# Optimization experiments

Hardware: AMD Instinct MI355X
Metric: run time of the kernel (lower is better)

Reference implementation:

```python
import jax, jax.numpy as jnp
import numpy as np

N = 100000
E = 640000
C = 128
NEG_SLOPE = 0.2


def _param(key, shape, scale=0.1):
    return jax.random.normal(key, shape, dtype=jnp.float32) * scale


def setup_inputs() -> dict:
    key = jax.random.key(0)
    ks = jax.random.split(key, 20)
    edge_index = jax.random.randint(ks[0], (2, E), 0, N, dtype=jnp.int32)
    emb = jax.random.normal(ks[1], (N, C), dtype=jnp.float32)  # node_embeddings.weight, a=1.0 normal
    d = {"edge_index": edge_index, "emb": emb}
    # per-layer GATv2Conv params: lin_l (W,b), lin_r (W,b), att vector, residual lin (no bias), out bias
    names = ["Wl", "bl", "Wr", "br", "att", "Wres", "bias"]
    shapes = [(C, C), (C,), (C, C), (C,), (C,), (C, C), (C,)]
    i = 2
    for layer in (1, 2):
        for nm, sh in zip(names, shapes):
            d[f"l{layer}_{nm}"] = _param(ks[i], sh)
            i += 1
    return d


def gatv2_layer(x, Wl, bl, Wr, br, att, Wres, bias, src, dst):
    # x: [N,C]; src/dst: [E+N] (self loops included)
    xl = x @ Wl.T + bl                       # source-side transform [N,C]
    xr = x @ Wr.T + br                       # target-side transform [N,C]
    m = jax.nn.leaky_relu(xl[src] + xr[dst], NEG_SLOPE)  # [E',C]
    e = m @ att                               # attention logits [E']
    emax = jax.ops.segment_max(e, dst, num_segments=N)
    ex = jnp.exp(e - emax[dst])
    denom = jax.ops.segment_sum(ex, dst, num_segments=N)
    alpha = ex / denom[dst]                   # segment softmax over incoming edges
    out = jax.ops.segment_sum(alpha[:, None] * xl[src], dst, num_segments=N)
    return out + x @ Wres.T + bias            # residual + bias


def reference(edge_index, emb,
              l1_Wl, l1_bl, l1_Wr, l1_br, l1_att, l1_Wres, l1_bias,
              l2_Wl, l2_bl, l2_Wr, l2_br, l2_att, l2_Wres, l2_bias):
    loops = jnp.arange(N, dtype=edge_index.dtype)
    src = jnp.concatenate([edge_index[0], loops])
    dst = jnp.concatenate([edge_index[1], loops])
    h = gatv2_layer(emb, l1_Wl, l1_bl, l1_Wr, l1_br, l1_att, l1_Wres, l1_bias, src, dst)
    h = jax.nn.relu(h)
    out = gatv2_layer(h, l2_Wl, l2_bl, l2_Wr, l2_br, l2_att, l2_Wres, l2_bias, src, dst)
    return out
```

## Files before the change

### kernel.cpp

```cpp
#include <hip/hip_runtime.h>
#include <math.h>

#define N_NODES 100000
#define N_EDGES 640000
#define C 128
#define NB_SCAN ((N_NODES + 255) / 256)

typedef __attribute__((ext_vector_type(8))) short short8;
typedef __attribute__((ext_vector_type(4))) float floatx4;
typedef __attribute__((ext_vector_type(2))) float float2v;
typedef unsigned int uint;
typedef unsigned short ushort;

__device__ __forceinline__ ushort f2bf(float f) {
    union { float f; uint u; } v; v.f = f;
    uint r = v.u + 0x7fffu + ((v.u >> 16) & 1u);
    return (ushort)(r >> 16);
}
__device__ __forceinline__ float2v upk2(uint u) {
    union { uint i; float f; } lo, hi;
    lo.i = u << 16; hi.i = u & 0xffff0000u;
    float2v r; r.x = lo.f; r.y = hi.f; return r;
}
__device__ __forceinline__ float2v fabs2(float2v v) {
    union { float2v f; uint u[2]; } a; a.f = v;
    a.u[0] &= 0x7fffffffu; a.u[1] &= 0x7fffffffu; return a.f;
}
__device__ __forceinline__ float2v fma2(float2v a, float2v b, float2v c) {
    return __builtin_elementwise_fma(a, b, c);
}

__global__ void hist_kernel(const int* __restrict__ ei, int* __restrict__ cnt,
                            ushort* __restrict__ slot) {
    int i = blockIdx.x * 256 + threadIdx.x;
    if (i >= N_EDGES) return;
    int d = ei[N_EDGES + i];
    slot[i] = (ushort)atomicAdd(&cnt[d], 1);
}

__global__ void scan_block(const int* __restrict__ cnt, int* __restrict__ row_off,
                           int* __restrict__ bsum) {
    __shared__ int s[256];
    int t = threadIdx.x, idx = blockIdx.x * 256 + t;
    int v = (idx < N_NODES) ? cnt[idx] : 0;
    s[t] = v;
    __syncthreads();
    #pragma unroll
    for (int off = 1; off < 256; off <<= 1) {
        int x = (t >= off) ? s[t - off] : 0;
        __syncthreads();
        s[t] += x;
        __syncthreads();
    }
    if (idx < N_NODES) row_off[idx] = s[t] - v;
    if (t == 255) bsum[blockIdx.x] = s[255];
}

__global__ void scan_tops(int* __restrict__ bsum) {
    __shared__ int s[512];
    int t = threadIdx.x;
    int v = (t < NB_SCAN) ? bsum[t] : 0;
    s[t] = v;
    __syncthreads();
    #pragma unroll
    for (int off = 1; off < 512; off <<= 1) {
        int x = (t >= off) ? s[t - off] : 0;
        __syncthreads();
        s[t] += x;
        __syncthreads();
    }
    if (t < NB_SCAN) bsum[t] = s[t] - v;
}

__global__ void add_off(int* __restrict__ row_off, const int* __restrict__ bsum) {
    int idx = blockIdx.x * 256 + threadIdx.x;
    if (idx < N_NODES) row_off[idx] += bsum[idx >> 8];
    if (idx == 0) row_off[N_NODES] = N_EDGES;
}

__global__ void scatter_kernel(const int* __restrict__ ei, const int* __restrict__ row_off,
                               const ushort* __restrict__ slot, int* __restrict__ colsrc) {
    int i = blockIdx.x * 256 + threadIdx.x;
    if (i >= N_EDGES) return;
    int d = ei[N_EDGES + i];
    colsrc[row_off[d] + (int)slot[i]] = ei[i];
}

__global__ void conv_w(const float* __restrict__ w0, const float* __restrict__ w1,
                       const float* __restrict__ w2, const float* __restrict__ w3,
                       const float* __restrict__ w4, const float* __restrict__ w5,
                       ushort* __restrict__ out) {
    int t = blockIdx.x * 256 + threadIdx.x;
    int m = t >> 11;
    int off = (t & 2047) * 8;
    const float* src = (m == 0) ? w0 : (m == 1) ? w1 : (m == 2) ? w2
                      : (m == 3) ? w3 : (m == 4) ? w4 : w5;
    float4 v0 = *(const float4*)(src + off);
    float4 v1 = *(const float4*)(src + off + 4);
    ushort tmp[8];
    tmp[0] = f2bf(v0.x); tmp[1] = f2bf(v0.y); tmp[2] = f2bf(v0.z); tmp[3] = f2bf(v0.w);
    tmp[4] = f2bf(v1.x); tmp[5] = f2bf(v1.y); tmp[6] = f2bf(v1.z); tmp[7] = f2bf(v1.w);
    *(uint4*)(out + (size_t)m * 16384 + off) = *(uint4*)tmp;
}

template <int IN_F32>
__global__ __launch_bounds__(512)
void gemm3_mfma(const void* __restrict__ xin,
                const ushort* __restrict__ wb,
                const float* __restrict__ bl, const float* __restrict__ br,
                const float* __restrict__ bres,
                ushort* __restrict__ xl, ushort* __restrict__ xr,
                ushort* __restrict__ res) {
    __shared__ ushort xs[64][136];
    const int tid = threadIdx.x;
    const int wave = tid >> 6, lane = tid & 63;
    const int quad = lane >> 4, l16 = lane & 15;
    const int n0 = blockIdx.x * 64;

    short8 bfr[3][4];
    const int col = wave * 16 + l16;
    #pragma unroll
    for (int ws = 0; ws < 3; ++ws)
        #pragma unroll
        for (int ks = 0; ks < 4; ++ks)
            bfr[ws][ks] = *(const short8*)(wb + (size_t)ws * 16384 + col * 128 + ks * 32 + quad * 8);

    {
        const int node = tid >> 3;
        const int kc = (tid & 7) * 16;
        const int n = n0 + node;
        ushort tmp[16];
        if (n < N_NODES) {
            if (IN_F32) {
                const float* src = (const float*)xin + (size_t)n * C + kc;
                float4 v[4];
                #pragma unroll
                for (int i = 0; i < 4; ++i) v[i] = ((const float4*)src)[i];
                #pragma unroll
                for (int i = 0; i < 4; ++i) {
                    tmp[i * 4 + 0] = f2bf(v[i].x); tmp[i * 4 + 1] = f2bf(v[i].y);
                    tmp[i * 4 + 2] = f2bf(v[i].z); tmp[i * 4 + 3] = f2bf(v[i].w);
                }
            } else {
                const ushort* src = (const ushort*)xin + (size_t)n * C + kc;
                *(uint4*)&tmp[0] = *(const uint4*)src;
                *(uint4*)&tmp[8] = *(const uint4*)(src + 8);
            }
        } else {
            #pragma unroll
            for (int i = 0; i < 16; ++i) tmp[i] = 0;
        }
        *(uint4*)&xs[node][kc]     = *(uint4*)&tmp[0];
        *(uint4*)&xs[node][kc + 8] = *(uint4*)&tmp[8];
    }
    __syncthreads();

    floatx4 acc[4][3];
    #pragma unroll
    for (int rt = 0; rt < 4; ++rt)
        #pragma unroll
        for (int ws = 0; ws < 3; ++ws)
            acc[rt][ws] = (floatx4){0.f, 0.f, 0.f, 0.f};

    #pragma unroll
    for (int rt = 0; rt < 4; ++rt) {
        short8 a[4];
        #pragma unroll
        for (int ks = 0; ks < 4; ++ks)
            a[ks] = *(const short8*)&xs[rt * 16 + l16][ks * 32 + quad * 8];
        #pragma unroll
        for (int ws = 0; ws < 3; ++ws)
            #pragma unroll
            for (int ks = 0; ks < 4; ++ks)
                acc[rt][ws] = __builtin_amdgcn_mfma_f32_16x16x32_bf16(a[ks], bfr[ws][ks], acc[rt][ws], 0, 0, 0);
    }

    float bias[3] = { bl[col], br[col], bres[col] };
    ushort* Os[3] = { xl, xr, res };
    #pragma unroll
    for (int ws = 0; ws < 3; ++ws)
        #pragma unroll
        for (int rt = 0; rt < 4; ++rt)
            #pragma unroll
            for (int r = 0; r < 4; ++r) {
                int row = n0 + rt * 16 + quad * 4 + r;
                if (row < N_NODES)
                    Os[ws][(size_t)row * C + col] = f2bf(acc[rt][ws][r] + bias[ws]);
            }
}

template <int OUT_BF16, int RELU>
__global__ __launch_bounds__(256)
void node_kernel(const ushort* __restrict__ xl, const ushort* __restrict__ xr,
                 const float* __restrict__ att, const int* __restrict__ row_off,
                 const int* __restrict__ colsrc,
                 const ushort* __restrict__ resin, void* __restrict__ outp) {
    const int tid = threadIdx.x;
    const int gl = tid & 15;
    const int base_c = gl * 8;
    const int d = blockIdx.x * 16 + (tid >> 4);

    float4 at0 = *(const float4*)(att + base_c);
    float4 at1 = *(const float4*)(att + base_c + 4);
    float2v a06[4], a04[4];
    a06[0] = (float2v){0.6f * at0.x, 0.6f * at0.y};
    a06[1] = (float2v){0.6f * at0.z, 0.6f * at0.w};
    a06[2] = (float2v){0.6f * at1.x, 0.6f * at1.y};
    a06[3] = (float2v){0.6f * at1.z, 0.6f * at1.w};
    a04[0] = (float2v){0.4f * at0.x, 0.4f * at0.y};
    a04[1] = (float2v){0.4f * at0.z, 0.4f * at0.w};
    a04[2] = (float2v){0.4f * at1.x, 0.4f * at1.y};
    a04[3] = (float2v){0.4f * at1.z, 0.4f * at1.w};

    uint4 uxr = *(const uint4*)(xr + (size_t)d * C + base_c);
    float2v xr2[4] = { upk2(uxr.x), upk2(uxr.y), upk2(uxr.z), upk2(uxr.w) };

    const int start = row_off[d];
    const int end   = row_off[d + 1];

    uint4 selfraw = *(const uint4*)(xl + (size_t)d * C + base_c);
    int pidx = (start < end) ? start : 0;
    int psrc = colsrc[pidx];
    uint4 raw = *(const uint4*)(xl + (size_t)psrc * C + base_c);

    float S;
    float2v O2[4];

    {
        float2v xv[4] = { upk2(selfraw.x), upk2(selfraw.y), upk2(selfraw.z), upk2(selfraw.w) };
        float2v m0 = xv[0] + xr2[0];
        float2v m1 = xv[1] + xr2[1];
        float2v m2 = xv[2] + xr2[2];
        float2v m3 = xv[3] + xr2[3];
        float2v pa = fma2(a06[0], m0, a04[0] * fabs2(m0));
        float2v pb = fma2(a06[1], m1, a04[1] * fabs2(m1));
        pa = fma2(a06[2], m2, fma2(a04[2], fabs2(m2), pa));
        pb = fma2(a06[3], m3, fma2(a04[3], fabs2(m3), pb));
        pa += pb;
        float p = pa.x + pa.y;
        #pragma unroll
        for (int off = 1; off < 16; off <<= 1) p += __shfl_xor(p, off, 64);
        const float w = __expf(p);
        S = w;
        float2v w2 = (float2v){w, w};
        #pragma unroll
        for (int j = 0; j < 4; ++j) O2[j] = w2 * xv[j];
    }

    for (int e = start; e < end; ++e) {
        const uint4 cur = raw;
        int nidx = (e + 1 < end) ? (e + 1) : start;
        int nsrc = colsrc[nidx];
        raw = *(const uint4*)(xl + (size_t)nsrc * C + base_c);

        float2v xv[4] = { upk2(cur.x), upk2(cur.y), upk2(cur.z), upk2(cur.w) };
        float2v m0 = xv[0] + xr2[0];
        float2v m1 = xv[1] + xr2[1];
        float2v m2 = xv[2] + xr2[2];
        float2v m3 = xv[3] + xr2[3];
        float2v pa = fma2(a06[0], m0, a04[0] * fabs2(m0));
        float2v pb = fma2(a06[1], m1, a04[1] * fabs2(m1));
        pa = fma2(a06[2], m2, fma2(a04[2], fabs2(m2), pa));
        pb = fma2(a06[3], m3, fma2(a04[3], fabs2(m3), pb));
        pa += pb;
        float p = pa.x + pa.y;
        #pragma unroll
        for (int off = 1; off < 16; off <<= 1) p += __shfl_xor(p, off, 64);
        const float w = __expf(p);
        S += w;
        float2v w2 = (float2v){w, w};
        #pragma unroll
        for (int j = 0; j < 4; ++j) O2[j] = fma2(w2, xv[j], O2[j]);
    }

    const float inv = 1.f / S;
    uint4 urs = *(const uint4*)(resin + (size_t)d * C + base_c);
    float2v rs[4] = { upk2(urs.x), upk2(urs.y), upk2(urs.z), upk2(urs.w) };
    float2v iv = (float2v){inv, inv};
    float r[8];
    #pragma unroll
    for (int j = 0; j < 4; ++j) {
        float2v rr = fma2(O2[j], iv, rs[j]);
        if (RELU) { rr.x = fmaxf(rr.x, 0.f); rr.y = fmaxf(rr.y, 0.f); }
        r[2 * j] = rr.x; r[2 * j + 1] = rr.y;
    }
    if (OUT_BF16) {
        ushort tmp[8];
        #pragma unroll
        for (int c = 0; c < 8; ++c) tmp[c] = f2bf(r[c]);
        *((uint4*)((ushort*)outp + (size_t)d * C + base_c)) = *(uint4*)tmp;
    } else {
        float* op = (float*)outp + (size_t)d * C + base_c;
        *(float4*)op       = make_float4(r[0], r[1], r[2], r[3]);
        *(float4*)(op + 4) = make_float4(r[4], r[5], r[6], r[7]);
    }
}

extern "C" void kernel_launch(void* const* d_in, const int* in_sizes, int n_in,
                              void* d_out, int out_size, void* d_ws, size_t ws_size,
                              hipStream_t stream) {
    const int*   ei  = (const int*)d_in[0];
    const float* emb = (const float*)d_in[1];
    const float* L1[7];
    const float* L2[7];
    for (int i = 0; i < 7; ++i) L1[i] = (const float*)d_in[2 + i];
    for (int i = 0; i < 7; ++i) L2[i] = (const float*)d_in[9 + i];
    float* out = (float*)d_out;

    const size_t NC = (size_t)N_NODES * C;
    ushort* xl  = (ushort*)d_ws;
    ushort* xr  = xl + NC;
    ushort* h   = xr + NC;
    ushort* r2  = h + NC;
    ushort* wb  = r2 + NC;
    int* row_off = (int*)(wb + 6 * 16384);
    int* bsum    = row_off + (N_NODES + 2);
    int* cnt     = bsum + 512;
    int* colsrc  = cnt + N_NODES;
    ushort* slot = (ushort*)(colsrc + N_EDGES);

    hipMemsetAsync(cnt, 0, N_NODES * sizeof(int), stream);
    hist_kernel<<<(N_EDGES + 255) / 256, 256, 0, stream>>>(ei, cnt, slot);
    scan_block<<<NB_SCAN, 256, 0, stream>>>(cnt, row_off, bsum);
    scan_tops<<<1, 512, 0, stream>>>(bsum);
    add_off<<<NB_SCAN, 256, 0, stream>>>(row_off, bsum);
    scatter_kernel<<<(N_EDGES + 255) / 256, 256, 0, stream>>>(ei, row_off, slot, colsrc);

    conv_w<<<48, 256, 0, stream>>>(L1[0], L1[2], L1[5], L2[0], L2[2], L2[5], wb);

    const int gblocks = (N_NODES + 63) / 64;
    const int nblocks = N_NODES / 16;

    gemm3_mfma<1><<<gblocks, 512, 0, stream>>>(emb, wb, L1[1], L1[3], L1[6], xl, xr, h);
    node_kernel<1, 1><<<nblocks, 256, 0, stream>>>(xl, xr, L1[4], row_off, colsrc, h, h);

    gemm3_mfma<0><<<gblocks, 512, 0, stream>>>(h, wb + 3 * 16384, L2[1], L2[3], L2[6], xl, xr, r2);
    node_kernel<0, 0><<<nblocks, 256, 0, stream>>>(xl, xr, L2[4], row_off, colsrc, r2, out);
}
```

Baseline: 344.2 us.

## Process multiple node tiles per GEMM block with double-buffered LDS prefetch

```diff
diff --git a/kernel.cpp b/kernel.cpp
--- a/kernel.cpp
+++ b/kernel.cpp
@@ -5,6 +5,8 @@
 #define N_EDGES 640000
 #define C 128
 #define NB_SCAN ((N_NODES + 255) / 256)
+#define TILES_PB 3
+#define N_TILES ((N_NODES + 63) / 64)
 
 typedef __attribute__((ext_vector_type(8))) short short8;
 typedef __attribute__((ext_vector_type(4))) float floatx4;
@@ -105,31 +107,34 @@
 
 template <int IN_F32>
 __global__ __launch_bounds__(512)
-void gemm3_mfma(const void* __restrict__ xin,
+void gemm3_pipe(const void* __restrict__ xin,
                 const ushort* __restrict__ wb,
                 const float* __restrict__ bl, const float* __restrict__ br,
                 const float* __restrict__ bres,
                 ushort* __restrict__ xl, ushort* __restrict__ xr,
                 ushort* __restrict__ res) {
-    __shared__ ushort xs[64][136];
+    __shared__ ushort xs[2][64][136];
     const int tid = threadIdx.x;
     const int wave = tid >> 6, lane = tid & 63;
     const int quad = lane >> 4, l16 = lane & 15;
-    const int n0 = blockIdx.x * 64;
+    const int col = wave * 16 + l16;
+    const int node = tid >> 3;
+    const int kc = (tid & 7) * 16;
 
     short8 bfr[3][4];
-    const int col = wave * 16 + l16;
     #pragma unroll
     for (int ws = 0; ws < 3; ++ws)
         #pragma unroll
         for (int ks = 0; ks < 4; ++ks)
-            bfr[ws][ks] = *(const short8*)(wb + (size_t)ws * 16384 + col * 128 + ks * 32 + quad * 8);
-
-    {
-        const int node = tid >> 3;
-        const int kc = (tid & 7) * 16;
-        const int n = n0 + node;
-        ushort tmp[16];
+            bfr[ws][ks] = *(const short8*)(wb + (size_t)ws * 16384 + (size_t)col * 128 + ks * 32 + quad * 8);
+
+    const float bias[3] = { bl[col], br[col], bres[col] };
+    ushort* const Os[3] = { xl, xr, res };
+
+    const int t0 = blockIdx.x * TILES_PB;
+
+    auto load_tile = [&](int tile, ushort* tmp) {
+        const int n = tile * 64 + node;
         if (n < N_NODES) {
             if (IN_F32) {
                 const float* src = (const float*)xin + (size_t)n * C + kc;
@@ -150,43 +155,57 @@
             #pragma unroll
             for (int i = 0; i < 16; ++i) tmp[i] = 0;
         }
-        *(uint4*)&xs[node][kc]     = *(uint4*)&tmp[0];
-        *(uint4*)&xs[node][kc + 8] = *(uint4*)&tmp[8];
-    }
-    __syncthreads();
-
-    floatx4 acc[4][3];
-    #pragma unroll
-    for (int rt = 0; rt < 4; ++rt)
+    };
+
+    ushort stg[16];
+    load_tile(t0, stg);
+    *(uint4*)&xs[0][node][kc]     = *(uint4*)&stg[0];
+    *(uint4*)&xs[0][node][kc + 8] = *(uint4*)&stg[8];
+
+    for (int i = 0; i < TILES_PB; ++i) {
+        const int tile = t0 + i;
+        __syncthreads();
+
+        const bool more = (i + 1 < TILES_PB);
+        if (more) load_tile(tile + 1, stg);
+
+        floatx4 acc[4][3];
+        #pragma unroll
+        for (int rt = 0; rt < 4; ++rt)
+            #pragma unroll
+            for (int ws = 0; ws < 3; ++ws)
+                acc[rt][ws] = (floatx4){0.f, 0.f, 0.f, 0.f};
+
+        #pragma unroll
+        for (int rt = 0; rt < 4; ++rt) {
+            short8 a[4];
+            #pragma unroll
+            for (int ks = 0; ks < 4; ++ks)
+                a[ks] = *(const short8*)&xs[i & 1][rt * 16 + l16][ks * 32 + quad * 8];
+            #pragma unroll
+            for (int ws = 0; ws < 3; ++ws)
+                #pragma unroll
+                for (int ks = 0; ks < 4; ++ks)
+                    acc[rt][ws] = __builtin_amdgcn_mfma_f32_16x16x32_bf16(a[ks], bfr[ws][ks], acc[rt][ws], 0, 0, 0);
+        }
+
+        if (more) {
+            *(uint4*)&xs[(i + 1) & 1][node][kc]     = *(uint4*)&stg[0];
+            *(uint4*)&xs[(i + 1) & 1][node][kc + 8] = *(uint4*)&stg[8];
+        }
+
+        const int n0 = tile * 64;
         #pragma unroll
         for (int ws = 0; ws < 3; ++ws)
-            acc[rt][ws] = (floatx4){0.f, 0.f, 0.f, 0.f};
-
-    #pragma unroll
-    for (int rt = 0; rt < 4; ++rt) {
-        short8 a[4];
-        #pragma unroll
-        for (int ks = 0; ks < 4; ++ks)
-            a[ks] = *(const short8*)&xs[rt * 16 + l16][ks * 32 + quad * 8];
-        #pragma unroll
-        for (int ws = 0; ws < 3; ++ws)
-            #pragma unroll
-            for (int ks = 0; ks < 4; ++ks)
-                acc[rt][ws] = __builtin_amdgcn_mfma_f32_16x16x32_bf16(a[ks], bfr[ws][ks], acc[rt][ws], 0, 0, 0);
-    }
-
-    float bias[3] = { bl[col], br[col], bres[col] };
-    ushort* Os[3] = { xl, xr, res };
-    #pragma unroll
-    for (int ws = 0; ws < 3; ++ws)
-        #pragma unroll
-        for (int rt = 0; rt < 4; ++rt)
-            #pragma unroll
-            for (int r = 0; r < 4; ++r) {
-                int row = n0 + rt * 16 + quad * 4 + r;
-                if (row < N_NODES)
-                    Os[ws][(size_t)row * C + col] = f2bf(acc[rt][ws][r] + bias[ws]);
-            }
+            #pragma unroll
+            for (int rt = 0; rt < 4; ++rt)
+                #pragma unroll
+                for (int r = 0; r < 4; ++r) {
+                    int row = n0 + rt * 16 + quad * 4 + r;
+                    if (row < N_NODES)
+                        Os[ws][(size_t)row * C + col] = f2bf(acc[rt][ws][r] + bias[ws]);
+                }
+    }
 }
 
 template <int OUT_BF16, int RELU>
@@ -328,12 +347,12 @@
 
     conv_w<<<48, 256, 0, stream>>>(L1[0], L1[2], L1[5], L2[0], L2[2], L2[5], wb);
 
-    const int gblocks = (N_NODES + 63) / 64;
+    const int gblocks = (N_TILES + TILES_PB - 1) / TILES_PB;
     const int nblocks = N_NODES / 16;
 
-    gemm3_mfma<1><<<gblocks, 512, 0, stream>>>(emb, wb, L1[1], L1[3], L1[6], xl, xr, h);
+    gemm3_pipe<1><<<gblocks, 512, 0, stream>>>(emb, wb, L1[1], L1[3], L1[6], xl, xr, h);
     node_kernel<1, 1><<<nblocks, 256, 0, stream>>>(xl, xr, L1[4], row_off, colsrc, h, h);
 
-    gemm3_mfma<0><<<gblocks, 512, 0, stream>>>(h, wb + 3 * 16384, L2[1], L2[3], L2[6], xl, xr, r2);
+    gemm3_pipe<0><<<gblocks, 512, 0, stream>>>(h, wb + 3 * 16384, L2[1], L2[3], L2[6], xl, xr, r2);
     node_kernel<0, 0><<<nblocks, 256, 0, stream>>>(xl, xr, L2[4], row_off, colsrc, r2, out);
 }
```

Result: faster. 327.7 us (-4.8%).
